# Kernel optimization log

Measured on AMD Instinct MI355X. Metric: run time of the kernel, lower is better.

Reference implementation:

```python
import jax, jax.numpy as jnp
import numpy as np

N_NODES = 50000
N_EDGES = 800000
IN_DIM = 128
HID = 128
OUT_DIM = 40
N_LAYERS = 4
N_GRAPHS = 128
BN_EPS = 1e-5


def setup_inputs() -> dict:
    key = jax.random.key(0)
    ks = jax.random.split(key, 12)
    sc1 = 1.0 / np.sqrt(HID)
    inp = {
        "x": jax.random.normal(ks[0], (N_NODES, IN_DIM), jnp.float32),
        "edge_index": jax.random.randint(ks[1], (2, N_EDGES), 0, N_NODES, jnp.int64),
        "batch": jnp.sort(jax.random.randint(ks[2], (N_NODES,), 0, N_GRAPHS, jnp.int64)),
        "W1s": jax.random.normal(ks[3], (N_LAYERS, IN_DIM, HID), jnp.float32) * sc1,
        "b1s": jnp.zeros((N_LAYERS, HID), jnp.float32),
        "W2s": jax.random.normal(ks[4], (N_LAYERS, HID, HID), jnp.float32) * sc1,
        "b2s": jnp.zeros((N_LAYERS, HID), jnp.float32),
        "gammas": jnp.ones((N_LAYERS, HID), jnp.float32),
        "betas": jnp.zeros((N_LAYERS, HID), jnp.float32),
        "bn_means": jax.random.normal(ks[5], (N_LAYERS, HID), jnp.float32) * 0.1,
        "bn_vars": jax.random.uniform(ks[6], (N_LAYERS, HID), jnp.float32, 0.5, 1.5),
        "eps_arr": jnp.zeros((N_LAYERS,), jnp.float32),
        "lin1_W": jax.random.normal(ks[7], (HID, HID), jnp.float32) * sc1,
        "lin1_b": jnp.zeros((HID,), jnp.float32),
        "lin2_W": jax.random.normal(ks[8], (HID, OUT_DIM), jnp.float32) * sc1,
        "lin2_b": jnp.zeros((OUT_DIM,), jnp.float32),
    }
    return inp


def _gin_forward(x, edge_index, batch, W1s, b1s, W2s, b2s, gammas, betas,
                 bn_means, bn_vars, eps_arr, lin1_W, lin1_b, lin2_W, lin2_b):
    src, dst = edge_index[0], edge_index[1]
    n = x.shape[0]
    for i in range(N_LAYERS):
        # GINConv: MLP((1+eps)*x_i + sum_{j->i} x_j)
        agg = jax.ops.segment_sum(x[src], dst, num_segments=n)  # [N, d]
        h = (1.0 + eps_arr[i]) * x + agg
        h = jax.nn.relu(h @ W1s[i] + b1s[i])
        h = jax.nn.relu(h @ W2s[i] + b2s[i])
        # BatchNorm1d (inference: running stats)
        x = gammas[i] * (h - bn_means[i]) * jax.lax.rsqrt(bn_vars[i] + BN_EPS) + betas[i]
    # global mean pool per graph
    sums = jax.ops.segment_sum(x, batch, num_segments=N_GRAPHS)  # [G, HID]
    counts = jax.ops.segment_sum(jnp.ones((n,), x.dtype), batch, num_segments=N_GRAPHS)
    pooled = sums / jnp.maximum(counts, 1.0)[:, None]
    h = jax.nn.relu(pooled @ lin1_W + lin1_b)
    # dropout is identity in eval mode
    logits = h @ lin2_W + lin2_b
    return jax.nn.log_softmax(logits, axis=-1)


def reference(x, edge_index, batch, W1s, b1s, W2s, b2s, gammas, betas,
              bn_means, bn_vars, eps_arr, lin1_W, lin1_b, lin2_W, lin2_b):
    return _gin_forward(x, edge_index, batch, W1s, b1s, W2s, b2s, gammas, betas,
                        bn_means, bn_vars, eps_arr, lin1_W, lin1_b, lin2_W, lin2_b)
```

## Files before the change

### kernel.cpp

```cpp
#include <hip/hip_runtime.h>
#include <hip/hip_bf16.h>
#include <math.h>

#define N_NODES  50000
#define N_EDGES  800000
#define HID      128
#define OUT_DIM  40
#define N_LAYERS 4
#define N_GRAPHS 128
#define BN_EPS   1e-5f
#define TROWS    32
#define LSTRIDE  136
#define CAP      64

typedef short v8s __attribute__((ext_vector_type(8)));
typedef float v4f __attribute__((ext_vector_type(4)));

static __device__ __forceinline__ short f2bf(float f) {
    __hip_bfloat16 h = __float2bfloat16(f);
    return __builtin_bit_cast(short, h);
}
static __device__ __forceinline__ float bflo(unsigned u) {
    return __builtin_bit_cast(float, u << 16);
}
static __device__ __forceinline__ float bfhi(unsigned u) {
    return __builtin_bit_cast(float, u & 0xffff0000u);
}
static __device__ __forceinline__ unsigned packbf(float a0, float a1) {
    return ((unsigned)(unsigned short)f2bf(a1) << 16) | (unsigned)(unsigned short)f2bf(a0);
}

__global__ __launch_bounds__(256) void k_pre(const float* __restrict__ x,
                                             unsigned* __restrict__ xb,
                                             const int* __restrict__ src,
                                             const int* __restrict__ dst,
                                             int* __restrict__ cursor,
                                             unsigned short* __restrict__ csr,
                                             const float* __restrict__ W1s,
                                             const float* __restrict__ W2s,
                                             const float* __restrict__ lin1,
                                             const float* __restrict__ lin2,
                                             short* __restrict__ Wp) {
    int b = blockIdx.x, t = threadIdx.x;
    if (b < 782) {
        int base = b * 1024;
#pragma unroll
        for (int k = 0; k < 4; k++) {
            int e = base + t + k * 256;
            if (e < N_EDGES) {
                int d = dst[e];
                int p = atomicAdd(&cursor[d], 1);
                if (p < CAP) csr[d * CAP + p] = (unsigned short)src[e];
            }
        }
    } else if (b < 3907) {
        int j = (b - 782) * 256 + t;
        const float4* x4 = (const float4*)x;
        float4 f0 = x4[2 * j];
        float4 f1 = x4[2 * j + 1];
        uint4 o;
        o.x = packbf(f0.x, f0.y);
        o.y = packbf(f0.z, f0.w);
        o.z = packbf(f1.x, f1.y);
        o.w = packbf(f1.z, f1.w);
        ((uint4*)xb)[j] = o;
    } else {
        int bp = b - 3907;
        if (bp < 9) {
            const float* W = (bp < 4) ? (W1s + bp * 16384)
                           : (bp < 8) ? (W2s + (bp - 4) * 16384)
                                      : lin1;
            short* o = Wp + (size_t)bp * 16384;
#pragma unroll
            for (int i = 0; i < 8; i++) {
                int c = i * 256 + t;
                int f = c >> 6, lane = c & 63;
                int ks = f >> 3, nt = f & 7;
                int k0 = ks * 32 + (lane >> 4) * 8;
                int n  = nt * 16 + (lane & 15);
                union { v8s v; short s[8]; } u;
#pragma unroll
                for (int j = 0; j < 8; j++) u.s[j] = f2bf(W[(k0 + j) * 128 + n]);
                *(v8s*)(o + (size_t)c * 8) = u.v;
            }
        } else {
            short* o = Wp + (size_t)9 * 16384;
#pragma unroll
            for (int i = 0; i < 3; i++) {
                int c = i * 256 + t;
                if (c < 768) {
                    int f = c >> 6, lane = c & 63;
                    int ks = f / 3, nt = f % 3;
                    int k0 = ks * 32 + (lane >> 4) * 8;
                    int n  = nt * 16 + (lane & 15);
                    union { v8s v; short s[8]; } u;
#pragma unroll
                    for (int j = 0; j < 8; j++)
                        u.s[j] = (n < OUT_DIM) ? f2bf(lin2[(k0 + j) * OUT_DIM + n]) : (short)0;
                    *(v8s*)(o + (size_t)(ks * 8 + nt) * 8 * 64 + (size_t)lane * 8) = u.v;
                }
            }
        }
    }
}

__global__ __launch_bounds__(256) void k_mlp(const short* __restrict__ xb,
                                             const unsigned short* __restrict__ csr,
                                             const int* __restrict__ deg,
                                             const short* __restrict__ Wp1,
                                             const short* __restrict__ Wp2,
                                             const float* __restrict__ b1,
                                             const float* __restrict__ b2,
                                             const float* __restrict__ gamma,
                                             const float* __restrict__ beta,
                                             const float* __restrict__ mean,
                                             const float* __restrict__ var,
                                             const float* __restrict__ eps_arr,
                                             int layer,
                                             short* __restrict__ out,
                                             int N) {
    __shared__ short H[TROWS * LSTRIDE];
    int tid = threadIdx.x, lane = tid & 63, w = tid >> 6;
    int m16 = lane & 15, quad = lane >> 4;
    int rbase = blockIdx.x * TROWS;

    {
        float sc = 1.0f + eps_arr[layer];
        const unsigned* X = (const unsigned*)xb;
        unsigned* Hu = (unsigned*)H;
        for (int i = w; i < TROWS; i += 4) {
            int r = rbase + i;
            unsigned pk = 0;
            if (r < N) {
                int cnt = min(deg[r], CAP);
                unsigned su = X[(size_t)r * 64 + lane];
                float a0 = sc * bflo(su), a1 = sc * bfhi(su);
                int idx = (lane < cnt) ? (int)csr[r * CAP + lane] : 0;
                int j = 0;
                for (; j + 8 <= cnt; j += 8) {
                    int s0 = __shfl(idx, j, 64),     s1 = __shfl(idx, j + 1, 64);
                    int s2 = __shfl(idx, j + 2, 64), s3 = __shfl(idx, j + 3, 64);
                    int s4 = __shfl(idx, j + 4, 64), s5 = __shfl(idx, j + 5, 64);
                    int s6 = __shfl(idx, j + 6, 64), s7 = __shfl(idx, j + 7, 64);
                    unsigned u0 = X[(size_t)s0 * 64 + lane];
                    unsigned u1 = X[(size_t)s1 * 64 + lane];
                    unsigned u2 = X[(size_t)s2 * 64 + lane];
                    unsigned u3 = X[(size_t)s3 * 64 + lane];
                    unsigned u4 = X[(size_t)s4 * 64 + lane];
                    unsigned u5 = X[(size_t)s5 * 64 + lane];
                    unsigned u6 = X[(size_t)s6 * 64 + lane];
                    unsigned u7 = X[(size_t)s7 * 64 + lane];
                    a0 += bflo(u0) + bflo(u1) + bflo(u2) + bflo(u3)
                        + bflo(u4) + bflo(u5) + bflo(u6) + bflo(u7);
                    a1 += bfhi(u0) + bfhi(u1) + bfhi(u2) + bfhi(u3)
                        + bfhi(u4) + bfhi(u5) + bfhi(u6) + bfhi(u7);
                }
                if (j + 4 <= cnt) {
                    int s0 = __shfl(idx, j, 64),     s1 = __shfl(idx, j + 1, 64);
                    int s2 = __shfl(idx, j + 2, 64), s3 = __shfl(idx, j + 3, 64);
                    unsigned u0 = X[(size_t)s0 * 64 + lane];
                    unsigned u1 = X[(size_t)s1 * 64 + lane];
                    unsigned u2 = X[(size_t)s2 * 64 + lane];
                    unsigned u3 = X[(size_t)s3 * 64 + lane];
                    a0 += bflo(u0) + bflo(u1) + bflo(u2) + bflo(u3);
                    a1 += bfhi(u0) + bfhi(u1) + bfhi(u2) + bfhi(u3);
                    j += 4;
                }
                for (; j < cnt; j++) {
                    int s = __shfl(idx, j, 64);
                    unsigned u = X[(size_t)s * 64 + lane];
                    a0 += bflo(u);
                    a1 += bfhi(u);
                }
                pk = packbf(a0, a1);
            }
            Hu[i * (LSTRIDE / 2) + lane] = pk;
        }
    }
    __syncthreads();

    float pb1[2], pb2[2], ps[2], pt[2];
#pragma unroll
    for (int nt = 0; nt < 2; nt++) {
        int c = w * 32 + nt * 16 + m16;
        pb1[nt] = b1[c];
        pb2[nt] = b2[c];
        float g = gamma[c];
        float iv = rsqrtf(var[c] + BN_EPS);
        ps[nt] = g * iv;
        pt[nt] = beta[c] - g * mean[c] * iv;
    }

    v4f acc[2][2];
#pragma unroll
    for (int mt = 0; mt < 2; mt++)
#pragma unroll
        for (int nt = 0; nt < 2; nt++) acc[mt][nt] = {0.f, 0.f, 0.f, 0.f};

#pragma unroll
    for (int ks = 0; ks < 4; ks++) {
        v8s bfr[2];
#pragma unroll
        for (int nt = 0; nt < 2; nt++)
            bfr[nt] = ((const v8s*)Wp1)[(ks * 8 + w * 2 + nt) * 64 + lane];
#pragma unroll
        for (int mt = 0; mt < 2; mt++) {
            v8s a = *(const v8s*)&H[(mt * 16 + m16) * LSTRIDE + ks * 32 + quad * 8];
#pragma unroll
            for (int nt = 0; nt < 2; nt++)
                acc[mt][nt] = __builtin_amdgcn_mfma_f32_16x16x32_bf16(a, bfr[nt], acc[mt][nt], 0, 0, 0);
        }
    }
    __syncthreads();

#pragma unroll
    for (int mt = 0; mt < 2; mt++)
#pragma unroll
        for (int nt = 0; nt < 2; nt++)
#pragma unroll
            for (int r4 = 0; r4 < 4; r4++) {
                float y = fmaxf(acc[mt][nt][r4] + pb1[nt], 0.f);
                H[(mt * 16 + quad * 4 + r4) * LSTRIDE + w * 32 + nt * 16 + m16] = f2bf(y);
            }
    __syncthreads();

    v4f acc2[2][2];
#pragma unroll
    for (int mt = 0; mt < 2; mt++)
#pragma unroll
        for (int nt = 0; nt < 2; nt++) acc2[mt][nt] = {0.f, 0.f, 0.f, 0.f};

#pragma unroll
    for (int ks = 0; ks < 4; ks++) {
        v8s bfr[2];
#pragma unroll
        for (int nt = 0; nt < 2; nt++)
            bfr[nt] = ((const v8s*)Wp2)[(ks * 8 + w * 2 + nt) * 64 + lane];
#pragma unroll
        for (int mt = 0; mt < 2; mt++) {
            v8s a = *(const v8s*)&H[(mt * 16 + m16) * LSTRIDE + ks * 32 + quad * 8];
#pragma unroll
            for (int nt = 0; nt < 2; nt++)
                acc2[mt][nt] = __builtin_amdgcn_mfma_f32_16x16x32_bf16(a, bfr[nt], acc2[mt][nt], 0, 0, 0);
        }
    }

#pragma unroll
    for (int mt = 0; mt < 2; mt++)
#pragma unroll
        for (int r4 = 0; r4 < 4; r4++) {
            int row = rbase + mt * 16 + quad * 4 + r4;
            if (row < N) {
#pragma unroll
                for (int nt = 0; nt < 2; nt++) {
                    float y = fmaxf(acc2[mt][nt][r4] + pb2[nt], 0.f);
                    y = ps[nt] * y + pt[nt];
                    out[(size_t)row * HID + w * 32 + nt * 16 + m16] = f2bf(y);
                }
            }
        }
}

__global__ __launch_bounds__(256) void k_pool(const short* __restrict__ Xs,
                                              const int* __restrict__ batch,
                                              short* __restrict__ pooled) {
    int g = blockIdx.x;
    int tid = threadIdx.x, lane = tid & 63, w = tid >> 6;
    __shared__ int sh[2];
    __shared__ float red0[256], red1[256];
    if (tid < 2) {
        int target = g + tid;
        int lo = 0, hi = N_NODES;
        while (lo < hi) {
            int mid = (lo + hi) >> 1;
            if (batch[mid] < target) lo = mid + 1; else hi = mid;
        }
        sh[tid] = lo;
    }
    __syncthreads();
    int lo = sh[0], hi = sh[1];
    const unsigned* X = (const unsigned*)Xs;
    float a0 = 0.f, a1 = 0.f;
    for (int r = lo + w; r < hi; r += 4) {
        unsigned u = X[(size_t)r * 64 + lane];
        a0 += bflo(u);
        a1 += bfhi(u);
    }
    red0[tid] = a0;
    red1[tid] = a1;
    __syncthreads();
    if (w == 0) {
        float s0 = red0[lane] + red0[64 + lane] + red0[128 + lane] + red0[192 + lane];
        float s1 = red1[lane] + red1[64 + lane] + red1[128 + lane] + red1[192 + lane];
        float c = fmaxf((float)(hi - lo), 1.0f);
        ((unsigned*)pooled)[g * 64 + lane] = packbf(s0 / c, s1 / c);
    }
}

__global__ __launch_bounds__(256) void k_head(const short* __restrict__ pooled,
                                              const short* __restrict__ Wp8,
                                              const short* __restrict__ Wp9,
                                              const float* __restrict__ b1h,
                                              const float* __restrict__ b2h,
                                              float* __restrict__ out) {
    __shared__ short Hl[128 * LSTRIDE];
    __shared__ float Ll[128 * OUT_DIM];
    int tid = threadIdx.x, lane = tid & 63, w = tid >> 6;
    int m16 = lane & 15, quad = lane >> 4;

    {
        int nh = w & 1, mh = w >> 1, base = mh * 64;
        float pb[4];
#pragma unroll
        for (int nt = 0; nt < 4; nt++) pb[nt] = b1h[nh * 64 + nt * 16 + m16];
        v4f acc[4][4];
#pragma unroll
        for (int mt = 0; mt < 4; mt++)
#pragma unroll
            for (int nt = 0; nt < 4; nt++) acc[mt][nt] = {0.f, 0.f, 0.f, 0.f};
#pragma unroll
        for (int ks = 0; ks < 4; ks++) {
            v8s bfr[4];
#pragma unroll
            for (int nt = 0; nt < 4; nt++)
                bfr[nt] = ((const v8s*)Wp8)[(ks * 8 + nh * 4 + nt) * 64 + lane];
#pragma unroll
            for (int mt = 0; mt < 4; mt++) {
                v8s a = *(const v8s*)(pooled + (size_t)(base + mt * 16 + m16) * HID
                                      + ks * 32 + quad * 8);
#pragma unroll
                for (int nt = 0; nt < 4; nt++)
                    acc[mt][nt] = __builtin_amdgcn_mfma_f32_16x16x32_bf16(a, bfr[nt], acc[mt][nt], 0, 0, 0);
            }
        }
#pragma unroll
        for (int mt = 0; mt < 4; mt++)
#pragma unroll
            for (int r4 = 0; r4 < 4; r4++) {
                int row = base + mt * 16 + quad * 4 + r4;
#pragma unroll
                for (int nt = 0; nt < 4; nt++)
                    Hl[row * LSTRIDE + nh * 64 + nt * 16 + m16] =
                        f2bf(fmaxf(acc[mt][nt][r4] + pb[nt], 0.f));
            }
    }
    __syncthreads();

    {
        v4f acc[2][3];
#pragma unroll
        for (int mt = 0; mt < 2; mt++)
#pragma unroll
            for (int nt = 0; nt < 3; nt++) acc[mt][nt] = {0.f, 0.f, 0.f, 0.f};
#pragma unroll
        for (int ks = 0; ks < 4; ks++) {
            v8s bfr[3];
#pragma unroll
            for (int nt = 0; nt < 3; nt++)
                bfr[nt] = ((const v8s*)Wp9)[(ks * 8 + nt) * 64 + lane];
#pragma unroll
            for (int mt = 0; mt < 2; mt++) {
                v8s a = *(const v8s*)&Hl[(w * 32 + mt * 16 + m16) * LSTRIDE + ks * 32 + quad * 8];
#pragma unroll
                for (int nt = 0; nt < 3; nt++)
                    acc[mt][nt] = __builtin_amdgcn_mfma_f32_16x16x32_bf16(a, bfr[nt], acc[mt][nt], 0, 0, 0);
            }
        }
#pragma unroll
        for (int mt = 0; mt < 2; mt++)
#pragma unroll
            for (int r4 = 0; r4 < 4; r4++) {
                int row = w * 32 + mt * 16 + quad * 4 + r4;
#pragma unroll
                for (int nt = 0; nt < 3; nt++) {
                    int col = nt * 16 + m16;
                    if (col < OUT_DIM)
                        Ll[row * OUT_DIM + col] = acc[mt][nt][r4] + b2h[col];
                }
            }
    }
    __syncthreads();

    for (int g = w; g < N_GRAPHS; g += 4) {
        float a = (lane < OUT_DIM) ? Ll[g * OUT_DIM + lane] : -INFINITY;
        float v = a;
        for (int d = 32; d > 0; d >>= 1) v = fmaxf(v, __shfl_xor(v, d, 64));
        float ex = (lane < OUT_DIM) ? expf(a - v) : 0.0f;
        float s = ex;
        for (int d = 32; d > 0; d >>= 1) s += __shfl_xor(s, d, 64);
        if (lane < OUT_DIM) out[g * OUT_DIM + lane] = a - v - logf(s);
    }
}

extern "C" void kernel_launch(void* const* d_in, const int* in_sizes, int n_in,
                              void* d_out, int out_size, void* d_ws, size_t ws_size,
                              hipStream_t stream) {
    const float* x       = (const float*)d_in[0];
    const int*   edge    = (const int*)d_in[1];
    const int*   batch   = (const int*)d_in[2];
    const float* W1s     = (const float*)d_in[3];
    const float* b1s     = (const float*)d_in[4];
    const float* W2s     = (const float*)d_in[5];
    const float* b2s     = (const float*)d_in[6];
    const float* gammas  = (const float*)d_in[7];
    const float* betas   = (const float*)d_in[8];
    const float* bn_m    = (const float*)d_in[9];
    const float* bn_v    = (const float*)d_in[10];
    const float* eps_arr = (const float*)d_in[11];
    const float* lin1_W  = (const float*)d_in[12];
    const float* lin1_b  = (const float*)d_in[13];
    const float* lin2_W  = (const float*)d_in[14];
    const float* lin2_b  = (const float*)d_in[15];

    const int* src = edge;
    const int* dst = edge + N_EDGES;

    short* bufA    = (short*)d_ws;
    short* bufB    = bufA + (size_t)N_NODES * HID;
    short* Wp      = bufB + (size_t)N_NODES * HID;
    short* pooled  = Wp + 10 * 16384;
    int*   cursor  = (int*)(pooled + N_GRAPHS * HID);
    unsigned short* csr = (unsigned short*)(cursor + N_NODES);

    hipMemsetAsync(cursor, 0, N_NODES * sizeof(int), stream);
    k_pre<<<3917, 256, 0, stream>>>(x, (unsigned*)bufA, src, dst, cursor, csr,
                                    W1s, W2s, lin1_W, lin2_W, Wp);

    const int mlpBlocks = (N_NODES + TROWS - 1) / TROWS;
    short* in   = bufA;
    short* outb = bufB;
    for (int l = 0; l < N_LAYERS; l++) {
        k_mlp<<<mlpBlocks, 256, 0, stream>>>(in, csr, cursor,
                                             Wp + (size_t)l * 16384,
                                             Wp + (size_t)(4 + l) * 16384,
                                             b1s + l * HID, b2s + l * HID,
                                             gammas + l * HID, betas + l * HID,
                                             bn_m + l * HID, bn_v + l * HID,
                                             eps_arr, l, outb, N_NODES);
        short* tmp = in; in = outb; outb = tmp;
    }

    k_pool<<<N_GRAPHS, 256, 0, stream>>>(in, batch, pooled);
    k_head<<<1, 256, 0, stream>>>(pooled, Wp + (size_t)8 * 16384, Wp + (size_t)9 * 16384,
                                  lin1_b, lin2_b, (float*)d_out);
}
```

Before: 335.1 us.

## Halve MLP row tile to 16 rows and reorder preprocessing with nontemporal loads

Result: slower. 375.5 us (+12.1%).

```diff
diff --git a/kernel.cpp b/kernel.cpp
--- a/kernel.cpp
+++ b/kernel.cpp
@@ -9,12 +9,14 @@
 #define N_LAYERS 4
 #define N_GRAPHS 128
 #define BN_EPS   1e-5f
-#define TROWS    32
+#define TROWS    16
 #define LSTRIDE  136
 #define CAP      64
 
 typedef short v8s __attribute__((ext_vector_type(8)));
 typedef float v4f __attribute__((ext_vector_type(4)));
+typedef float cv4f __attribute__((ext_vector_type(4)));
+typedef unsigned v4u __attribute__((ext_vector_type(4)));
 
 static __device__ __forceinline__ short f2bf(float f) {
     __hip_bfloat16 h = __float2bfloat16(f);
@@ -42,30 +44,19 @@
                                              const float* __restrict__ lin2,
                                              short* __restrict__ Wp) {
     int b = blockIdx.x, t = threadIdx.x;
-    if (b < 782) {
-        int base = b * 1024;
-#pragma unroll
-        for (int k = 0; k < 4; k++) {
-            int e = base + t + k * 256;
-            if (e < N_EDGES) {
-                int d = dst[e];
-                int p = atomicAdd(&cursor[d], 1);
-                if (p < CAP) csr[d * CAP + p] = (unsigned short)src[e];
-            }
-        }
-    } else if (b < 3907) {
-        int j = (b - 782) * 256 + t;
-        const float4* x4 = (const float4*)x;
-        float4 f0 = x4[2 * j];
-        float4 f1 = x4[2 * j + 1];
-        uint4 o;
+    if (b < 3125) {
+        int j = b * 256 + t;
+        const cv4f* x4 = (const cv4f*)x;
+        cv4f f0 = __builtin_nontemporal_load(&x4[2 * j]);
+        cv4f f1 = __builtin_nontemporal_load(&x4[2 * j + 1]);
+        v4u o;
         o.x = packbf(f0.x, f0.y);
         o.y = packbf(f0.z, f0.w);
         o.z = packbf(f1.x, f1.y);
         o.w = packbf(f1.z, f1.w);
-        ((uint4*)xb)[j] = o;
-    } else {
-        int bp = b - 3907;
+        __builtin_nontemporal_store(o, &((v4u*)xb)[j]);
+    } else if (b < 3135) {
+        int bp = b - 3125;
         if (bp < 9) {
             const float* W = (bp < 4) ? (W1s + bp * 16384)
                            : (bp < 8) ? (W2s + (bp - 4) * 16384)
@@ -99,6 +90,18 @@
                         u.s[j] = (n < OUT_DIM) ? f2bf(lin2[(k0 + j) * OUT_DIM + n]) : (short)0;
                     *(v8s*)(o + (size_t)(ks * 8 + nt) * 8 * 64 + (size_t)lane * 8) = u.v;
                 }
+            }
+        }
+    } else {
+        int base = (b - 3135) * 1024;
+#pragma unroll
+        for (int k = 0; k < 4; k++) {
+            int e = base + t + k * 256;
+            if (e < N_EDGES) {
+                int d = __builtin_nontemporal_load(&dst[e]);
+                int s = __builtin_nontemporal_load(&src[e]);
+                int p = atomicAdd(&cursor[d], 1);
+                if (p < CAP) csr[d * CAP + p] = (unsigned short)s;
             }
         }
     }
@@ -191,11 +194,9 @@
         pt[nt] = beta[c] - g * mean[c] * iv;
     }
 
-    v4f acc[2][2];
-#pragma unroll
-    for (int mt = 0; mt < 2; mt++)
-#pragma unroll
-        for (int nt = 0; nt < 2; nt++) acc[mt][nt] = {0.f, 0.f, 0.f, 0.f};
+    v4f acc[2];
+    acc[0] = {0.f, 0.f, 0.f, 0.f};
+    acc[1] = {0.f, 0.f, 0.f, 0.f};
 
 #pragma unroll
     for (int ks = 0; ks < 4; ks++) {
@@ -203,32 +204,25 @@
 #pragma unroll
         for (int nt = 0; nt < 2; nt++)
             bfr[nt] = ((const v8s*)Wp1)[(ks * 8 + w * 2 + nt) * 64 + lane];
-#pragma unroll
-        for (int mt = 0; mt < 2; mt++) {
-            v8s a = *(const v8s*)&H[(mt * 16 + m16) * LSTRIDE + ks * 32 + quad * 8];
-#pragma unroll
-            for (int nt = 0; nt < 2; nt++)
-                acc[mt][nt] = __builtin_amdgcn_mfma_f32_16x16x32_bf16(a, bfr[nt], acc[mt][nt], 0, 0, 0);
-        }
-    }
-    __syncthreads();
-
-#pragma unroll
-    for (int mt = 0; mt < 2; mt++)
+        v8s a = *(const v8s*)&H[m16 * LSTRIDE + ks * 32 + quad * 8];
 #pragma unroll
         for (int nt = 0; nt < 2; nt++)
-#pragma unroll
-            for (int r4 = 0; r4 < 4; r4++) {
-                float y = fmaxf(acc[mt][nt][r4] + pb1[nt], 0.f);
-                H[(mt * 16 + quad * 4 + r4) * LSTRIDE + w * 32 + nt * 16 + m16] = f2bf(y);
-            }
-    __syncthreads();
-
-    v4f acc2[2][2];
-#pragma unroll
-    for (int mt = 0; mt < 2; mt++)
-#pragma unroll
-        for (int nt = 0; nt < 2; nt++) acc2[mt][nt] = {0.f, 0.f, 0.f, 0.f};
+            acc[nt] = __builtin_amdgcn_mfma_f32_16x16x32_bf16(a, bfr[nt], acc[nt], 0, 0, 0);
+    }
+    __syncthreads();
+
+#pragma unroll
+    for (int nt = 0; nt < 2; nt++)
+#pragma unroll
+        for (int r4 = 0; r4 < 4; r4++) {
+            float y = fmaxf(acc[nt][r4] + pb1[nt], 0.f);
+            H[(quad * 4 + r4) * LSTRIDE + w * 32 + nt * 16 + m16] = f2bf(y);
+        }
+    __syncthreads();
+
+    v4f acc2[2];
+    acc2[0] = {0.f, 0.f, 0.f, 0.f};
+    acc2[1] = {0.f, 0.f, 0.f, 0.f};
 
 #pragma unroll
     for (int ks = 0; ks < 4; ks++) {
@@ -236,29 +230,24 @@
 #pragma unroll
         for (int nt = 0; nt < 2; nt++)
             bfr[nt] = ((const v8s*)Wp2)[(ks * 8 + w * 2 + nt) * 64 + lane];
-#pragma unroll
-        for (int mt = 0; mt < 2; mt++) {
-            v8s a = *(const v8s*)&H[(mt * 16 + m16) * LSTRIDE + ks * 32 + quad * 8];
-#pragma unroll
-            for (int nt = 0; nt < 2; nt++)
-                acc2[mt][nt] = __builtin_amdgcn_mfma_f32_16x16x32_bf16(a, bfr[nt], acc2[mt][nt], 0, 0, 0);
-        }
-    }
-
-#pragma unroll
-    for (int mt = 0; mt < 2; mt++)
-#pragma unroll
-        for (int r4 = 0; r4 < 4; r4++) {
-            int row = rbase + mt * 16 + quad * 4 + r4;
-            if (row < N) {
-#pragma unroll
-                for (int nt = 0; nt < 2; nt++) {
-                    float y = fmaxf(acc2[mt][nt][r4] + pb2[nt], 0.f);
-                    y = ps[nt] * y + pt[nt];
-                    out[(size_t)row * HID + w * 32 + nt * 16 + m16] = f2bf(y);
-                }
-            }
-        }
+        v8s a = *(const v8s*)&H[m16 * LSTRIDE + ks * 32 + quad * 8];
+#pragma unroll
+        for (int nt = 0; nt < 2; nt++)
+            acc2[nt] = __builtin_amdgcn_mfma_f32_16x16x32_bf16(a, bfr[nt], acc2[nt], 0, 0, 0);
+    }
+
+#pragma unroll
+    for (int r4 = 0; r4 < 4; r4++) {
+        int row = rbase + quad * 4 + r4;
+        if (row < N) {
+#pragma unroll
+            for (int nt = 0; nt < 2; nt++) {
+                float y = fmaxf(acc2[nt][r4] + pb2[nt], 0.f);
+                y = ps[nt] * y + pt[nt];
+                out[(size_t)row * HID + w * 32 + nt * 16 + m16] = f2bf(y);
+            }
+        }
+    }
 }
 
 __global__ __launch_bounds__(256) void k_pool(const short* __restrict__ Xs,
@@ -422,7 +411,7 @@
     int*   cursor  = (int*)(pooled + N_GRAPHS * HID);
     unsigned short* csr = (unsigned short*)(cursor + N_NODES);
 
-    hipMemsetAsync(cursor, 0, N_NODES * sizeof(int), stream);
+    (void)hipMemsetAsync(cursor, 0, N_NODES * sizeof(int), stream);
     k_pre<<<3917, 256, 0, stream>>>(x, (unsigned*)bufA, src, dst, cursor, csr,
                                     W1s, W2s, lin1_W, lin2_W, Wp);
 
```

## Fuse global mean pooling into last GIN layer via atomic accumulation

Applied to the files above, without the earlier changes.

Measured after the change: 368.8 us. +10.1%, slower.

```diff
diff --git a/kernel.cpp b/kernel.cpp
--- a/kernel.cpp
+++ b/kernel.cpp
@@ -118,6 +118,9 @@
                                              const float* __restrict__ eps_arr,
                                              int layer,
                                              short* __restrict__ out,
+                                             const int* __restrict__ batch,
+                                             float* __restrict__ pooledF,
+                                             int lastL,
                                              int N) {
     __shared__ short H[TROWS * LSTRIDE];
     int tid = threadIdx.x, lane = tid & 63, w = tid >> 6;
@@ -245,68 +248,88 @@
         }
     }
 
-#pragma unroll
-    for (int mt = 0; mt < 2; mt++)
-#pragma unroll
-        for (int r4 = 0; r4 < 4; r4++) {
-            int row = rbase + mt * 16 + quad * 4 + r4;
-            if (row < N) {
-#pragma unroll
-                for (int nt = 0; nt < 2; nt++) {
-                    float y = fmaxf(acc2[mt][nt][r4] + pb2[nt], 0.f);
-                    y = ps[nt] * y + pt[nt];
-                    out[(size_t)row * HID + w * 32 + nt * 16 + m16] = f2bf(y);
-                }
-            }
-        }
-}
-
-__global__ __launch_bounds__(256) void k_pool(const short* __restrict__ Xs,
+    if (!lastL) {
+#pragma unroll
+        for (int mt = 0; mt < 2; mt++)
+#pragma unroll
+            for (int r4 = 0; r4 < 4; r4++) {
+                int row = rbase + mt * 16 + quad * 4 + r4;
+                if (row < N) {
+#pragma unroll
+                    for (int nt = 0; nt < 2; nt++) {
+                        float y = fmaxf(acc2[mt][nt][r4] + pb2[nt], 0.f);
+                        y = ps[nt] * y + pt[nt];
+                        out[(size_t)row * HID + w * 32 + nt * 16 + m16] = f2bf(y);
+                    }
+                }
+            }
+    } else {
+        bool fast = (rbase + TROWS <= N) && (batch[rbase] == batch[rbase + TROWS - 1]);
+        if (fast) {
+            int g = batch[rbase];
+#pragma unroll
+            for (int nt = 0; nt < 2; nt++) {
+                float v = 0.f;
+#pragma unroll
+                for (int mt = 0; mt < 2; mt++)
+#pragma unroll
+                    for (int r4 = 0; r4 < 4; r4++) {
+                        float y = fmaxf(acc2[mt][nt][r4] + pb2[nt], 0.f);
+                        v += ps[nt] * y + pt[nt];
+                    }
+                v += __shfl_xor(v, 16, 64);
+                v += __shfl_xor(v, 32, 64);
+                if (quad == 0)
+                    atomicAdd(&pooledF[g * HID + w * 32 + nt * 16 + m16], v);
+            }
+        } else {
+#pragma unroll
+            for (int mt = 0; mt < 2; mt++)
+#pragma unroll
+                for (int r4 = 0; r4 < 4; r4++) {
+                    int row = rbase + mt * 16 + quad * 4 + r4;
+                    if (row < N) {
+                        int g = batch[row];
+#pragma unroll
+                        for (int nt = 0; nt < 2; nt++) {
+                            float y = fmaxf(acc2[mt][nt][r4] + pb2[nt], 0.f);
+                            y = ps[nt] * y + pt[nt];
+                            atomicAdd(&pooledF[g * HID + w * 32 + nt * 16 + m16], y);
+                        }
+                    }
+                }
+        }
+    }
+}
+
+__global__ __launch_bounds__(256) void k_head(const float* __restrict__ pooledF,
                                               const int* __restrict__ batch,
-                                              short* __restrict__ pooled) {
-    int g = blockIdx.x;
-    int tid = threadIdx.x, lane = tid & 63, w = tid >> 6;
-    __shared__ int sh[2];
-    __shared__ float red0[256], red1[256];
-    if (tid < 2) {
-        int target = g + tid;
-        int lo = 0, hi = N_NODES;
-        while (lo < hi) {
-            int mid = (lo + hi) >> 1;
-            if (batch[mid] < target) lo = mid + 1; else hi = mid;
-        }
-        sh[tid] = lo;
-    }
-    __syncthreads();
-    int lo = sh[0], hi = sh[1];
-    const unsigned* X = (const unsigned*)Xs;
-    float a0 = 0.f, a1 = 0.f;
-    for (int r = lo + w; r < hi; r += 4) {
-        unsigned u = X[(size_t)r * 64 + lane];
-        a0 += bflo(u);
-        a1 += bfhi(u);
-    }
-    red0[tid] = a0;
-    red1[tid] = a1;
-    __syncthreads();
-    if (w == 0) {
-        float s0 = red0[lane] + red0[64 + lane] + red0[128 + lane] + red0[192 + lane];
-        float s1 = red1[lane] + red1[64 + lane] + red1[128 + lane] + red1[192 + lane];
-        float c = fmaxf((float)(hi - lo), 1.0f);
-        ((unsigned*)pooled)[g * 64 + lane] = packbf(s0 / c, s1 / c);
-    }
-}
-
-__global__ __launch_bounds__(256) void k_head(const short* __restrict__ pooled,
                                               const short* __restrict__ Wp8,
                                               const short* __restrict__ Wp9,
                                               const float* __restrict__ b1h,
                                               const float* __restrict__ b2h,
                                               float* __restrict__ out) {
+    __shared__ short Al[128 * LSTRIDE];
     __shared__ short Hl[128 * LSTRIDE];
     __shared__ float Ll[128 * OUT_DIM];
+    __shared__ float invc[N_GRAPHS];
     int tid = threadIdx.x, lane = tid & 63, w = tid >> 6;
     int m16 = lane & 15, quad = lane >> 4;
+
+    if (tid < N_GRAPHS) {
+        int g = tid, lo = 0, hi = N_NODES;
+        while (lo < hi) { int m = (lo + hi) >> 1; if (batch[m] < g) lo = m + 1; else hi = m; }
+        int s = lo; lo = 0; hi = N_NODES;
+        while (lo < hi) { int m = (lo + hi) >> 1; if (batch[m] < g + 1) lo = m + 1; else hi = m; }
+        invc[g] = 1.0f / fmaxf((float)(lo - s), 1.0f);
+    }
+    __syncthreads();
+
+    for (int i = tid; i < N_GRAPHS * HID; i += 256) {
+        int row = i >> 7, col = i & 127;
+        Al[row * LSTRIDE + col] = f2bf(pooledF[i] * invc[row]);
+    }
+    __syncthreads();
 
     {
         int nh = w & 1, mh = w >> 1, base = mh * 64;
@@ -326,8 +349,7 @@
                 bfr[nt] = ((const v8s*)Wp8)[(ks * 8 + nh * 4 + nt) * 64 + lane];
 #pragma unroll
             for (int mt = 0; mt < 4; mt++) {
-                v8s a = *(const v8s*)(pooled + (size_t)(base + mt * 16 + m16) * HID
-                                      + ks * 32 + quad * 8);
+                v8s a = *(const v8s*)&Al[(base + mt * 16 + m16) * LSTRIDE + ks * 32 + quad * 8];
 #pragma unroll
                 for (int nt = 0; nt < 4; nt++)
                     acc[mt][nt] = __builtin_amdgcn_mfma_f32_16x16x32_bf16(a, bfr[nt], acc[mt][nt], 0, 0, 0);
@@ -418,11 +440,11 @@
     short* bufA    = (short*)d_ws;
     short* bufB    = bufA + (size_t)N_NODES * HID;
     short* Wp      = bufB + (size_t)N_NODES * HID;
-    short* pooled  = Wp + 10 * 16384;
-    int*   cursor  = (int*)(pooled + N_GRAPHS * HID);
-    unsigned short* csr = (unsigned short*)(cursor + N_NODES);
-
-    hipMemsetAsync(cursor, 0, N_NODES * sizeof(int), stream);
+    int*   cursor  = (int*)(Wp + 10 * 16384);
+    float* pooledF = (float*)(cursor + N_NODES);
+    unsigned short* csr = (unsigned short*)(pooledF + N_GRAPHS * HID);
+
+    (void)hipMemsetAsync(cursor, 0, (N_NODES + N_GRAPHS * HID) * sizeof(int), stream);
     k_pre<<<3917, 256, 0, stream>>>(x, (unsigned*)bufA, src, dst, cursor, csr,
                                     W1s, W2s, lin1_W, lin2_W, Wp);
 
@@ -430,17 +452,19 @@
     short* in   = bufA;
     short* outb = bufB;
     for (int l = 0; l < N_LAYERS; l++) {
+        int lastL = (l == N_LAYERS - 1) ? 1 : 0;
         k_mlp<<<mlpBlocks, 256, 0, stream>>>(in, csr, cursor,
                                              Wp + (size_t)l * 16384,
                                              Wp + (size_t)(4 + l) * 16384,
                                              b1s + l * HID, b2s + l * HID,
                                              gammas + l * HID, betas + l * HID,
                                              bn_m + l * HID, bn_v + l * HID,
-                                             eps_arr, l, outb, N_NODES);
+                                             eps_arr, l, outb, batch, pooledF,
+                                             lastL, N_NODES);
         short* tmp = in; in = outb; outb = tmp;
     }
 
-    k_pool<<<N_GRAPHS, 256, 0, stream>>>(in, batch, pooled);
-    k_head<<<1, 256, 0, stream>>>(pooled, Wp + (size_t)8 * 16384, Wp + (size_t)9 * 16384,
-                                  lin1_b, lin2_b, (float*)d_out);
-}
+    k_head<<<1, 256, 0, stream>>>(pooledF, batch, Wp + (size_t)8 * 16384,
+                                  Wp + (size_t)9 * 16384, lin1_b, lin2_b,
+                                  (float*)d_out);
+}
```
